# Performance work log

Hardware: AMD Instinct MI355X
Metric: run time of the kernel (lower is better)

Reference implementation:

```python
import jax, jax.numpy as jnp
import numpy as np

CAPACITY = 0.5


def setup_inputs() -> dict:
    key = jax.random.key(0)
    ks = jax.random.split(key, 5)
    b, s, d, dff = 4, 4096, 1024, 4096
    x = jax.random.normal(ks[0], (b, s, d), dtype=jnp.float32)
    attention_mask = jnp.ones((b, s), dtype=jnp.int32)
    Wr = jax.random.normal(ks[1], (d, 1), dtype=jnp.float32) * (1.0 / np.sqrt(d))
    br = jnp.zeros((1,), dtype=jnp.float32)
    W1 = jax.random.normal(ks[2], (d, dff), dtype=jnp.float32) * (1.0 / np.sqrt(d))
    b1 = jnp.zeros((dff,), dtype=jnp.float32)
    W2 = jax.random.normal(ks[3], (dff, d), dtype=jnp.float32) * (1.0 / np.sqrt(dff))
    b2 = jnp.zeros((d,), dtype=jnp.float32)
    return {"x": x, "attention_mask": attention_mask, "Wr": Wr, "br": br,
            "W1": W1, "b1": b1, "W2": W2, "b2": b2}


def _block(filtered_x, router_weights, W1, b1, W2, b2):
    # Stand-in MoD block: residual router-weighted GELU MLP.
    h = jax.nn.gelu(jnp.einsum('bkd,df->bkf', filtered_x, W1) + b1)
    out = jnp.einsum('bkf,fd->bkd', h, W2) + b2
    return filtered_x + router_weights * out  # router_weights: [b,k,1]


def reference(x, attention_mask, Wr, br, W1, b1, W2, b2):
    b, s, d = x.shape
    top_k = int(s * CAPACITY)
    router_logits = jnp.einsum('bsd,do->bso', x, Wr) + br        # [b,s,1]
    scores = jax.nn.sigmoid(router_logits[..., 0])               # [b,s]
    token_weights, token_index = jax.lax.top_k(scores, top_k)    # [b,k]
    sort_order = jnp.argsort(token_index, axis=1)                # positions
    sorted_indices = jnp.take_along_axis(token_index, sort_order, axis=1)  # [b,k]
    filtered_x = jnp.take_along_axis(x, sorted_indices[..., None], axis=1)  # [b,k,d]
    tw = jax.nn.softmax(token_weights, axis=1)                   # softmax over k
    router_weights = jnp.take_along_axis(tw, sort_order, axis=1)[..., None]  # [b,k,1]
    block_out = _block(filtered_x, router_weights, W1, b1, W2, b2)
    batch_idx = jnp.arange(b)[:, None]
    hidden_states = x.at[batch_idx, sorted_indices].set(block_out)
    # aux loss: BCE-with-logits, targets = 1 on selected tokens
    targets = jnp.zeros((b, s), dtype=x.dtype).at[batch_idx, sorted_indices].set(1.0)
    l = router_logits[..., 0]
    aux_loss = jnp.mean(jnp.maximum(l, 0.0) - l * targets + jnp.log1p(jnp.exp(-jnp.abs(l))))
    return hidden_states, aux_loss
```

## Files before the change

### kernel.cpp

```cpp
#include <hip/hip_runtime.h>

#define NB 4
#define SEQ 4096
#define DIM 1024
#define DFF 4096
#define KSEL 2048
#define NTOK (NB * SEQ)
#define MR (NB * KSEL)

typedef float f32x4_t __attribute__((ext_vector_type(4)));
typedef unsigned long u64_t;
typedef unsigned long u64x2_t __attribute__((ext_vector_type(2)));
typedef int i32x8_t __attribute__((ext_vector_type(8)));

__device__ __forceinline__ unsigned char f2fp8(float f) {
  return (unsigned char)(__builtin_amdgcn_cvt_pk_fp8_f32(f, f, 0, false) & 0xff);
}

__device__ __forceinline__ int kperm(int kb) {
  return ((kb >> 3) & 3) * 32 + (kb >> 5) * 8 + (kb & 7);
}

#define GLD16(g, l) __builtin_amdgcn_global_load_lds( \
    (const __attribute__((address_space(1))) void*)(g), \
    (__attribute__((address_space(3))) void*)(l), 16, 0, 0)

__global__ void prep_kernel(const float* __restrict__ W1, unsigned char* __restrict__ W1t,
                            const float* __restrict__ W2, unsigned char* __restrict__ W2t,
                            const float* __restrict__ x, const float* __restrict__ Wr,
                            const float* __restrict__ br,
                            float* __restrict__ logits, float* __restrict__ scores,
                            float* __restrict__ out) {
  __shared__ float tl[32][33];
  int bid = blockIdx.x;
  if (bid < 8192) {
    const float* W; unsigned char* Wt; int R, C, bx, by;
    if (bid < 4096) { W = W1; Wt = W1t; R = DIM; C = DFF; bx = bid & 127; by = bid >> 7; }
    else { bid -= 4096; W = W2; Wt = W2t; R = DFF; C = DIM; bx = bid & 31; by = bid >> 5; }
    int c0 = bx * 32;
    int r0 = by * 32;
    int tx = threadIdx.x & 31, ty = threadIdx.x >> 5;
#pragma unroll
    for (int i = 0; i < 4; ++i)
      tl[ty + i * 8][tx] = W[(size_t)(r0 + ty + i * 8) * C + c0 + tx];
    __syncthreads();
    int k = r0 + tx;
    int pos = (k & ~127) + kperm(k & 127);
#pragma unroll
    for (int i = 0; i < 4; ++i)
      Wt[(size_t)(c0 + ty + i * 8) * R + pos] = f2fp8(16.f * tl[tx][ty + i * 8]);
  } else {
    int lane = threadIdx.x & 63;
    int wid  = threadIdx.x >> 6;
    int row  = (bid - 8192) * 4 + wid;
    const float4* xr = (const float4*)(x + (size_t)row * DIM);
    float4* orow = (float4*)(out + (size_t)row * DIM);
    const float4* w4 = (const float4*)Wr;
    float sum = 0.f;
#pragma unroll
    for (int i = 0; i < 4; ++i) {
      float4 a = xr[lane + i * 64];
      float4 w = w4[lane + i * 64];
      orow[lane + i * 64] = a;
      sum += a.x * w.x + a.y * w.y + a.z * w.z + a.w * w.w;
    }
#pragma unroll
    for (int off = 32; off > 0; off >>= 1) sum += __shfl_down(sum, off);
    if (lane == 0) {
      float l = sum + br[0];
      logits[row] = l;
      scores[row] = 1.f / (1.f + expf(-l));
    }
  }
}

__global__ void rank_kernel(const float* __restrict__ scores, int* __restrict__ sel) {
  __shared__ float s_sc[SEQ];
  int batch = blockIdx.x >> 8;
  int chunk = blockIdx.x & 255;
  int t = threadIdx.x;
  const float4* sb4 = (const float4*)(scores + batch * SEQ);
  float4* ls4 = (float4*)s_sc;
#pragma unroll
  for (int i = 0; i < 4; ++i) ls4[t + i * 256] = sb4[t + i * 256];
  __syncthreads();
  int tok = chunk * 16 + (t >> 4);
  int sg  = t & 15;
  float s = s_sc[tok];
  const float4* seg = ls4 + sg * 64;
  int jbase = sg * 256;
  int rank = 0;
#pragma unroll 4
  for (int j4 = 0; j4 < 64; ++j4) {
    float4 v = seg[j4];
    int j = jbase + j4 * 4;
    rank += (v.x > s || (v.x == s && j     < tok)) ? 1 : 0;
    rank += (v.y > s || (v.y == s && j + 1 < tok)) ? 1 : 0;
    rank += (v.z > s || (v.z == s && j + 2 < tok)) ? 1 : 0;
    rank += (v.w > s || (v.w == s && j + 3 < tok)) ? 1 : 0;
  }
#pragma unroll
  for (int off = 8; off > 0; off >>= 1) rank += __shfl_down(rank, off, 16);
  if (sg == 0) sel[batch * SEQ + tok] = (rank < KSEL) ? 1 : 0;
}

__global__ void pack_kernel(const float* __restrict__ scores, const int* __restrict__ sel,
                            int* __restrict__ rows, float* __restrict__ rwv) {
  __shared__ float red[16];
  __shared__ int scn[1024];
  int batch = blockIdx.x;
  int t = threadIdx.x;
  const float* sb = scores + batch * SEQ;
  const int* fb = sel + batch * SEQ;
  float sc[4]; int fl[4];
#pragma unroll
  for (int i = 0; i < 4; ++i) { sc[i] = sb[t * 4 + i]; fl[i] = fb[t * 4 + i]; }
  float m = fmaxf(fmaxf(sc[0], sc[1]), fmaxf(sc[2], sc[3]));
#pragma unroll
  for (int off = 32; off > 0; off >>= 1) m = fmaxf(m, __shfl_down(m, off));
  if ((t & 63) == 0) red[t >> 6] = m;
  __syncthreads();
  if (t == 0) { float v = red[0]; for (int i = 1; i < 16; ++i) v = fmaxf(v, red[i]); red[0] = v; }
  __syncthreads();
  m = red[0];
  __syncthreads();
  float ex[4]; float esum = 0.f;
#pragma unroll
  for (int i = 0; i < 4; ++i) { ex[i] = expf(sc[i] - m); if (fl[i]) esum += ex[i]; }
#pragma unroll
  for (int off = 32; off > 0; off >>= 1) esum += __shfl_down(esum, off);
  if ((t & 63) == 0) red[t >> 6] = esum;
  __syncthreads();
  if (t == 0) { float v = 0.f; for (int i = 0; i < 16; ++i) v += red[i]; red[0] = v; }
  __syncthreads();
  float total = red[0];
  int cnt = fl[0] + fl[1] + fl[2] + fl[3];
  scn[t] = cnt;
  __syncthreads();
  for (int off = 1; off < 1024; off <<= 1) {
    int a = scn[t];
    int b = (t >= off) ? scn[t - off] : 0;
    __syncthreads();
    scn[t] = a + b;
    __syncthreads();
  }
  int p = scn[t] - cnt;
#pragma unroll
  for (int i = 0; i < 4; ++i) {
    if (fl[i]) {
      rows[batch * KSEL + p] = t * 4 + i;
      rwv[batch * KSEL + p]  = ex[i] / total;
      ++p;
    }
  }
}

__global__ void gather_kernel(const float* __restrict__ x, const int* __restrict__ rows,
                              unsigned char* __restrict__ Xc) {
  int mrow = blockIdx.x;
  int batch = mrow >> 11;
  int tok = rows[mrow];
  const float4* src = (const float4*)(x + ((size_t)(batch * SEQ + tok)) * DIM);
  int t = threadIdx.x;
  float4 v = src[t];
  unsigned lo = (unsigned)__builtin_amdgcn_cvt_pk_fp8_f32(v.x, v.y, 0, false);
  unsigned both = (unsigned)__builtin_amdgcn_cvt_pk_fp8_f32(v.z, v.w, (int)lo, true);
  int panel = mrow >> 7, rowp = mrow & 127;
  int k = t * 4;
  int pos = kperm(k & 127);
  size_t addr = (size_t)panel * (128 * DIM) + (size_t)(k >> 7) * 16384
              + (size_t)(pos >> 5) * 4096 + (size_t)rowp * 32 + (pos & 31);
  *(unsigned*)(Xc + addr) = both;
}

template <int EPI>
__global__ __launch_bounds__(256)
void gemm15(const unsigned char* __restrict__ A, const unsigned char* __restrict__ Bt,
            int M, int N, int K,
            const float* __restrict__ bias,
            unsigned char* __restrict__ Hout,
            const float* __restrict__ x,
            const int* __restrict__ rows,
            const float* __restrict__ rwv,
            float* __restrict__ out) {
  __shared__ __align__(16) unsigned char Bs[2][128 * 128];

  const int t = threadIdx.x;
  const int lane = t & 63;
  const int wid = t >> 6;
  const int wm = wid >> 1;
  const int wn = wid & 1;

  const int nwg = gridDim.x;
  const int qq = nwg >> 3;
  const int nid = (blockIdx.x & 7) * qq + (blockIdx.x >> 3);
  const int gx = N / 128;
  const int by = nid / gx;
  const int bx = nid - by * gx;
  const int bm0 = by * 128;
  const int bn0 = bx * 128;

  const size_t ldb = (size_t)K;
  const char* Bb = (const char*)Bt + (size_t)bn0 * ldb;

  const int srow = t >> 3;
  const size_t stage_off = (size_t)srow * ldb + (size_t)((((t & 7) ^ (srow & 7)) * 16));

  const int cbs0 = ((lane >> 4) * 32     ) ^ ((lane & 7) << 4);
  const int cbs1 = ((lane >> 4) * 32 + 16) ^ ((lane & 7) << 4);

  const char* Ap = (const char*)A + (size_t)by * 128 * (size_t)K + (size_t)(lane >> 4) * 4096;
  const char* arow[4];
#pragma unroll
  for (int i = 0; i < 4; ++i)
    arow[i] = Ap + (size_t)(wm * 64 + i * 16 + (lane & 15)) * 32;

  f32x4_t acc[4][4];
  f32x4_t zero = {0.f, 0.f, 0.f, 0.f};
#pragma unroll
  for (int i = 0; i < 4; ++i)
#pragma unroll
    for (int j = 0; j < 4; ++j) acc[i][j] = zero;

  const int NT = K / 128;

  i32x8_t amA[4], amB[4];

  auto loadA = [&](i32x8_t* am, int kt) {
#pragma unroll
    for (int i = 0; i < 4; ++i)
      am[i] = *(const i32x8_t*)(arow[i] + (size_t)kt * 16384);
  };
  auto stageB = [&](int buf, int kt) {
    const size_t kb = (size_t)kt * 128 + stage_off;
    char* dst = (char*)Bs[buf] + t * 16;
#pragma unroll
    for (int c = 0; c < 4; ++c)
      GLD16(Bb + kb + (size_t)(c * 32) * ldb, dst + c * 4096);
  };
  auto compute = [&](const i32x8_t* am, int buf) {
    i32x8_t bq[4];
#pragma unroll
    for (int j = 0; j < 4; ++j) {
      const char* bp = (const char*)Bs[buf] + (wn * 64 + j * 16 + (lane & 15)) * 128;
      union { u64x2_t q[2]; i32x8_t v; } u;
      u.q[0] = *(const u64x2_t*)(bp + cbs0);
      u.q[1] = *(const u64x2_t*)(bp + cbs1);
      bq[j] = u.v;
    }
    __builtin_amdgcn_s_setprio(1);
#pragma unroll
    for (int i = 0; i < 4; ++i)
#pragma unroll
      for (int j = 0; j < 4; ++j)
        acc[i][j] = __builtin_amdgcn_mfma_scale_f32_16x16x128_f8f6f4(
            am[i], bq[j], acc[i][j], 0, 0,
            0, 0x7f7f7f7f, 0, 0x7f7f7f7f);
    __builtin_amdgcn_s_setprio(0);
  };

  loadA(amA, 0);
  stageB(0, 0);

  for (int kt = 0; kt < NT; kt += 2) {
    loadA(amB, kt + 1);
    stageB(1, kt + 1);
    asm volatile("s_waitcnt vmcnt(8)" ::: "memory");
    __builtin_amdgcn_s_barrier();
    __builtin_amdgcn_sched_barrier(0);
    compute(amA, 0);
    __builtin_amdgcn_s_barrier();
    if (kt + 2 < NT) {
      loadA(amA, kt + 2);
      stageB(0, kt + 2);
      asm volatile("s_waitcnt vmcnt(8)" ::: "memory");
    } else {
      asm volatile("s_waitcnt vmcnt(0)" ::: "memory");
    }
    __builtin_amdgcn_s_barrier();
    __builtin_amdgcn_sched_barrier(0);
    compute(amB, 1);
    __builtin_amdgcn_s_barrier();
  }

  const int rb = (lane >> 4) * 4;
  const int cc = lane & 15;
#pragma unroll
  for (int i = 0; i < 4; ++i) {
#pragma unroll
    for (int qi = 0; qi < 4; ++qi) {
      int grow = bm0 + wm * 64 + i * 16 + rb + qi;
      if (EPI == 1) {
        int panel = grow >> 7, rowp = grow & 127;
#pragma unroll
        for (int j = 0; j < 4; ++j) {
          int gcol = bn0 + wn * 64 + j * 16 + cc;
          float v = acc[i][j][qi] * 0.0625f + bias[gcol];
          float cp = 0.7978845608028654f * (v + 0.044715f * v * v * v);
          float g = v / (1.f + __expf(-2.f * cp));
          int pos = kperm(gcol & 127);
          size_t addr = (size_t)panel * (128 * DFF) + (size_t)(gcol >> 7) * 16384
                      + (size_t)(pos >> 5) * 4096 + (size_t)rowp * 32 + (pos & 31);
          Hout[addr] = f2fp8(g);
        }
      } else {
        int batch = grow >> 11;
        int tok = rows[grow];
        float rw = rwv[grow];
        size_t obase = ((size_t)(batch * SEQ + tok)) * DIM;
#pragma unroll
        for (int j = 0; j < 4; ++j) {
          int gcol = bn0 + wn * 64 + j * 16 + cc;
          float v = acc[i][j][qi] * 0.0625f + bias[gcol];
          out[obase + gcol] = x[obase + gcol] + rw * v;
        }
      }
    }
  }
}

__global__ void aux_kernel(const float* __restrict__ logits, const int* __restrict__ sel,
                           float* __restrict__ out, int out_size) {
  __shared__ float red[16];
  int t = threadIdx.x;
  float sum = 0.f;
  for (int i = t; i < NTOK; i += 1024) {
    float l = logits[i];
    float tgt = sel[i] ? 1.f : 0.f;
    sum += fmaxf(l, 0.f) - l * tgt + log1pf(expf(-fabsf(l)));
  }
#pragma unroll
  for (int off = 32; off > 0; off >>= 1) sum += __shfl_down(sum, off);
  if ((t & 63) == 0) red[t >> 6] = sum;
  __syncthreads();
  if (t == 0) {
    float v = 0.f;
    for (int i = 0; i < 16; ++i) v += red[i];
    out[out_size - 1] = v / (float)NTOK;
  }
}

extern "C" void kernel_launch(void* const* d_in, const int* in_sizes, int n_in,
                              void* d_out, int out_size, void* d_ws, size_t ws_size,
                              hipStream_t stream) {
  const float* x  = (const float*)d_in[0];
  const float* Wr = (const float*)d_in[2];
  const float* br = (const float*)d_in[3];
  const float* W1 = (const float*)d_in[4];
  const float* b1 = (const float*)d_in[5];
  const float* W2 = (const float*)d_in[6];
  const float* b2 = (const float*)d_in[7];
  float* out = (float*)d_out;

  char* ws = (char*)d_ws;
  float* logits = (float*)(ws);
  float* scores = (float*)(ws + 65536);
  int*   sel    = (int*)(ws + 131072);
  int*   rows   = (int*)(ws + 196608);
  float* rwv    = (float*)(ws + 229376);
  unsigned char* W1t = (unsigned char*)(ws + 327680);
  unsigned char* W2t = (unsigned char*)(ws + 327680 + 4194304);
  unsigned char* Xc  = (unsigned char*)(ws + 327680 + 2 * 4194304);
  unsigned char* H   = (unsigned char*)(ws + 327680 + 2 * 4194304 + 8388608);

  prep_kernel<<<12288, 256, 0, stream>>>(W1, W1t, W2, W2t, x, Wr, br, logits, scores, out);
  rank_kernel<<<NTOK / 16, 256, 0, stream>>>(scores, sel);
  pack_kernel<<<NB, 1024, 0, stream>>>(scores, sel, rows, rwv);
  gather_kernel<<<MR, 256, 0, stream>>>(x, rows, Xc);
  gemm15<1><<<(MR / 128) * (DFF / 128), 256, 0, stream>>>(
      Xc, W1t, MR, DFF, DIM, b1, H, nullptr, nullptr, nullptr, nullptr);
  gemm15<2><<<(MR / 128) * (DIM / 128), 256, 0, stream>>>(
      H, W2t, MR, DIM, DFF, b2, nullptr, x, rows, rwv, out);
  aux_kernel<<<1, 1024, 0, stream>>>(logits, sel, out, out_size);
}
```

Before: 200.8 us.

## Fuse token gather with passthrough copy and deepen GEMM load pipeline

Before, the prep kernel copied every x row into the output, and a separate gather kernel re-read the selected rows. Now prep only computes router logits. A new per-token kernel reads each x row once and either writes it as fp8 into the packed GEMM input, via a new token-to-slot map from pack, or copies it to the output. This removes a redundant 64MB write for selected tokens and a second read of selected rows. The GEMM wait counter is also relaxed from 8 to 12 outstanding loads, allowing more in-flight prefetch; this relies on the load count per stage matching for correctness.

```diff
diff --git a/kernel.cpp b/kernel.cpp
--- a/kernel.cpp
+++ b/kernel.cpp
@@ -29,8 +29,7 @@
                             const float* __restrict__ W2, unsigned char* __restrict__ W2t,
                             const float* __restrict__ x, const float* __restrict__ Wr,
                             const float* __restrict__ br,
-                            float* __restrict__ logits, float* __restrict__ scores,
-                            float* __restrict__ out) {
+                            float* __restrict__ logits, float* __restrict__ scores) {
   __shared__ float tl[32][33];
   int bid = blockIdx.x;
   if (bid < 8192) {
@@ -54,14 +53,12 @@
     int wid  = threadIdx.x >> 6;
     int row  = (bid - 8192) * 4 + wid;
     const float4* xr = (const float4*)(x + (size_t)row * DIM);
-    float4* orow = (float4*)(out + (size_t)row * DIM);
     const float4* w4 = (const float4*)Wr;
     float sum = 0.f;
 #pragma unroll
     for (int i = 0; i < 4; ++i) {
       float4 a = xr[lane + i * 64];
       float4 w = w4[lane + i * 64];
-      orow[lane + i * 64] = a;
       sum += a.x * w.x + a.y * w.y + a.z * w.z + a.w * w.w;
     }
 #pragma unroll
@@ -105,7 +102,8 @@
 }
 
 __global__ void pack_kernel(const float* __restrict__ scores, const int* __restrict__ sel,
-                            int* __restrict__ rows, float* __restrict__ rwv) {
+                            int* __restrict__ rows, float* __restrict__ rwv,
+                            int* __restrict__ slot) {
   __shared__ float red[16];
   __shared__ int scn[1024];
   int batch = blockIdx.x;
@@ -150,32 +148,37 @@
     if (fl[i]) {
       rows[batch * KSEL + p] = t * 4 + i;
       rwv[batch * KSEL + p]  = ex[i] / total;
+      slot[batch * SEQ + t * 4 + i] = batch * KSEL + p;
       ++p;
     }
   }
 }
 
-__global__ void gather_kernel(const float* __restrict__ x, const int* __restrict__ rows,
-                              unsigned char* __restrict__ Xc) {
-  int mrow = blockIdx.x;
-  int batch = mrow >> 11;
-  int tok = rows[mrow];
-  const float4* src = (const float4*)(x + ((size_t)(batch * SEQ + tok)) * DIM);
+__global__ void gather_copy_kernel(const float* __restrict__ x, const int* __restrict__ sel,
+                                   const int* __restrict__ slot,
+                                   unsigned char* __restrict__ Xc, float* __restrict__ out) {
+  int tokg = blockIdx.x;
+  const float4* src = (const float4*)(x + (size_t)tokg * DIM);
   int t = threadIdx.x;
   float4 v = src[t];
-  unsigned lo = (unsigned)__builtin_amdgcn_cvt_pk_fp8_f32(v.x, v.y, 0, false);
-  unsigned both = (unsigned)__builtin_amdgcn_cvt_pk_fp8_f32(v.z, v.w, (int)lo, true);
-  int panel = mrow >> 7, rowp = mrow & 127;
-  int k = t * 4;
-  int pos = kperm(k & 127);
-  size_t addr = (size_t)panel * (128 * DIM) + (size_t)(k >> 7) * 16384
-              + (size_t)(pos >> 5) * 4096 + (size_t)rowp * 32 + (pos & 31);
-  *(unsigned*)(Xc + addr) = both;
+  if (sel[tokg]) {
+    unsigned lo = (unsigned)__builtin_amdgcn_cvt_pk_fp8_f32(v.x, v.y, 0, false);
+    unsigned both = (unsigned)__builtin_amdgcn_cvt_pk_fp8_f32(v.z, v.w, (int)lo, true);
+    int mrow = slot[tokg];
+    int panel = mrow >> 7, rowp = mrow & 127;
+    int k = t * 4;
+    int pos = kperm(k & 127);
+    size_t addr = (size_t)panel * (128 * DIM) + (size_t)(k >> 7) * 16384
+                + (size_t)(pos >> 5) * 4096 + (size_t)rowp * 32 + (pos & 31);
+    *(unsigned*)(Xc + addr) = both;
+  } else {
+    ((float4*)(out + (size_t)tokg * DIM))[t] = v;
+  }
 }
 
 template <int EPI>
 __global__ __launch_bounds__(256)
-void gemm15(const unsigned char* __restrict__ A, const unsigned char* __restrict__ Bt,
+void gemm16(const unsigned char* __restrict__ A, const unsigned char* __restrict__ Bt,
             int M, int N, int K,
             const float* __restrict__ bias,
             unsigned char* __restrict__ Hout,
@@ -265,7 +268,7 @@
   for (int kt = 0; kt < NT; kt += 2) {
     loadA(amB, kt + 1);
     stageB(1, kt + 1);
-    asm volatile("s_waitcnt vmcnt(8)" ::: "memory");
+    asm volatile("s_waitcnt vmcnt(12)" ::: "memory");
     __builtin_amdgcn_s_barrier();
     __builtin_amdgcn_sched_barrier(0);
     compute(amA, 0);
@@ -273,7 +276,7 @@
     if (kt + 2 < NT) {
       loadA(amA, kt + 2);
       stageB(0, kt + 2);
-      asm volatile("s_waitcnt vmcnt(8)" ::: "memory");
+      asm volatile("s_waitcnt vmcnt(12)" ::: "memory");
     } else {
       asm volatile("s_waitcnt vmcnt(0)" ::: "memory");
     }
@@ -358,18 +361,19 @@
   int*   sel    = (int*)(ws + 131072);
   int*   rows   = (int*)(ws + 196608);
   float* rwv    = (float*)(ws + 229376);
+  int*   slot   = (int*)(ws + 262144);
   unsigned char* W1t = (unsigned char*)(ws + 327680);
   unsigned char* W2t = (unsigned char*)(ws + 327680 + 4194304);
   unsigned char* Xc  = (unsigned char*)(ws + 327680 + 2 * 4194304);
   unsigned char* H   = (unsigned char*)(ws + 327680 + 2 * 4194304 + 8388608);
 
-  prep_kernel<<<12288, 256, 0, stream>>>(W1, W1t, W2, W2t, x, Wr, br, logits, scores, out);
+  prep_kernel<<<12288, 256, 0, stream>>>(W1, W1t, W2, W2t, x, Wr, br, logits, scores);
   rank_kernel<<<NTOK / 16, 256, 0, stream>>>(scores, sel);
-  pack_kernel<<<NB, 1024, 0, stream>>>(scores, sel, rows, rwv);
-  gather_kernel<<<MR, 256, 0, stream>>>(x, rows, Xc);
-  gemm15<1><<<(MR / 128) * (DFF / 128), 256, 0, stream>>>(
+  pack_kernel<<<NB, 1024, 0, stream>>>(scores, sel, rows, rwv, slot);
+  gather_copy_kernel<<<NTOK, 256, 0, stream>>>(x, sel, slot, Xc, out);
+  gemm16<1><<<(MR / 128) * (DFF / 128), 256, 0, stream>>>(
       Xc, W1t, MR, DFF, DIM, b1, H, nullptr, nullptr, nullptr, nullptr);
-  gemm15<2><<<(MR / 128) * (DIM / 128), 256, 0, stream>>>(
+  gemm16<2><<<(MR / 128) * (DIM / 128), 256, 0, stream>>>(
       H, W2t, MR, DIM, DFF, b2, nullptr, x, rows, rwv, out);
   aux_kernel<<<1, 1024, 0, stream>>>(logits, sel, out, out_size);
 }
```

Result: faster. 195.6 us (-2.6%).
